# Kernel optimization log

Hardware: AMD Instinct MI355X
Metric: run time of the kernel (lower is better)

Reference implementation:

```python
import jax, jax.numpy as jnp
import numpy as np

B, S, H, L, NH, OUT = 64, 512, 512, 2, 8, 1
HD = H // NH
SKIP_INTERVAL = 2
EPS = 1e-5


def ln(x, g, b):
    m = x.mean(-1, keepdims=True)
    v = x.var(-1, keepdims=True)
    return (x - m) / jnp.sqrt(v + EPS) * g + b


def setup_inputs() -> dict:
    key = jax.random.key(0)
    ks = iter(jax.random.split(key, 64))
    def nrm(shape, s=0.02):
        return jax.random.normal(next(ks), shape, jnp.float32) * s
    inp = {
        'x': jax.random.normal(next(ks), (B, S, H), jnp.float32),
        # stacked per-layer LSTM params (input_size == hidden_size == H)
        'Wi': nrm((L, 4 * H, H)), 'bi': jnp.zeros((L, 4 * H), jnp.float32).at[:, H:2 * H].set(1.0),
        'Wh': nrm((L, 4 * H, H)), 'bh': jnp.zeros((L, 4 * H), jnp.float32).at[:, H:2 * H].set(1.0),
        'g_in': jnp.ones((L, 4 * H), jnp.float32), 'b_in': jnp.zeros((L, 4 * H), jnp.float32),
        'g_hid': jnp.ones((L, 4 * H), jnp.float32), 'b_hid': jnp.zeros((L, 4 * H), jnp.float32),
        'g_cell': jnp.ones((L, H), jnp.float32), 'b_cell': jnp.zeros((L, H), jnp.float32),
        # highway per layer
        'hw_Wt': nrm((L, H, H)), 'hw_bt': jnp.zeros((L, H), jnp.float32),
        'hw_Wc': nrm((L, H, H)), 'hw_bc': jnp.full((L, H), -1.0, jnp.float32),
        'hw_Wh': nrm((L, H, H)), 'hw_bh': jnp.zeros((L, H), jnp.float32),
        # attention
        'Wq': nrm((H, H)), 'bq': jnp.zeros((H,), jnp.float32),
        'Wk': nrm((H, H)), 'bk': jnp.zeros((H,), jnp.float32),
        'Wv': nrm((H, H)), 'bv': jnp.zeros((H,), jnp.float32),
        'Wo': nrm((H, H)), 'bo': jnp.zeros((H,), jnp.float32),
        'att_g': jnp.ones((H,), jnp.float32), 'att_b': jnp.zeros((H,), jnp.float32),
        # output norm + projection head
        'on_g': jnp.ones((H,), jnp.float32), 'on_b': jnp.zeros((H,), jnp.float32),
        'Wp1': nrm((H // 2, H)), 'bp1': jnp.zeros((H // 2,), jnp.float32),
        'Wp2': nrm((OUT, H // 2)), 'bp2': jnp.zeros((OUT,), jnp.float32),
    }
    return inp


def _forward(x, Wi, bi, Wh, bh, g_in, b_in, g_hid, b_hid, g_cell, b_cell,
             hw_Wt, hw_bt, hw_Wc, hw_bc, hw_Wh, hw_bh,
             Wq, bq, Wk, bk, Wv, bv, Wo, bo, att_g, att_b,
             on_g, on_b, Wp1, bp1, Wp2, bp2):
    def lstm_layer(seq, l):
        # precompute input projection + its LayerNorm for all timesteps: [B,S,4H]
        ip = ln(jnp.einsum('bsh,gh->bsg', seq, Wi[l]) + bi[l], g_in[l], b_in[l])
        def step(carry, ip_t):
            h, c = carry
            hp = ln(h @ Wh[l].T + bh[l], g_hid[l], b_hid[l])
            i_, f_, g_, o_ = jnp.split(ip_t + hp, 4, axis=-1)
            c = jax.nn.sigmoid(f_) * c + jax.nn.sigmoid(i_) * jnp.tanh(g_)
            h = jax.nn.sigmoid(o_) * jnp.tanh(ln(c, g_cell[l], b_cell[l]))
            return (h, c), h
        h0 = jnp.zeros((seq.shape[0], H), seq.dtype)
        _, hs = jax.lax.scan(step, (h0, h0), jnp.swapaxes(ip, 0, 1))
        return jnp.swapaxes(hs, 0, 1)  # [B,S,H]

    seq = x
    for l in range(L):
        h_seq = lstm_layer(seq, l)
        # highway network
        tg = jax.nn.sigmoid(h_seq @ hw_Wt[l].T + hw_bt[l])
        cg = jax.nn.sigmoid(h_seq @ hw_Wc[l].T + hw_bc[l])
        tr = jax.nn.relu(h_seq @ hw_Wh[l].T + hw_bh[l])
        h_seq = tg * tr + cg * h_seq
        # skip connection every SKIP_INTERVAL layers
        if l > 0 and (l + 1) % SKIP_INTERVAL == 0:
            h_seq = h_seq + seq
        seq = h_seq

    # multi-head self-attention with residual + LayerNorm
    def heads(y):
        return jnp.swapaxes(y.reshape(B, S, NH, HD), 1, 2)  # [B,NH,S,HD]
    q = heads(seq @ Wq.T + bq)
    k = heads(seq @ Wk.T + bk)
    v = heads(seq @ Wv.T + bv)
    scale = 1.0 / float(np.sqrt(HD))
    scores = jnp.einsum('bnqd,bnkd->bnqk', q, k) * scale
    aw = jax.nn.softmax(scores, axis=-1)
    ctx = jnp.einsum('bnqk,bnkd->bnqd', aw, v)
    ctx = jnp.swapaxes(ctx, 1, 2).reshape(B, S, H)
    att = ln(ctx @ Wo.T + bo + seq, att_g, att_b)

    # last timestep -> output norm -> MLP head
    last = ln(att[:, -1], on_g, on_b)
    hmid = jax.nn.relu(last @ Wp1.T + bp1)
    return hmid @ Wp2.T + bp2  # [B, OUT]


def reference(x, Wi, bi, Wh, bh, g_in, b_in, g_hid, b_hid, g_cell, b_cell,
              hw_Wt, hw_bt, hw_Wc, hw_bc, hw_Wh, hw_bh,
              Wq, bq, Wk, bk, Wv, bv, Wo, bo, att_g, att_b,
              on_g, on_b, Wp1, bp1, Wp2, bp2):
    return _forward(x, Wi, bi, Wh, bh, g_in, b_in, g_hid, b_hid, g_cell, b_cell,
                    hw_Wt, hw_bt, hw_Wc, hw_bc, hw_Wh, hw_bh,
                    Wq, bq, Wk, bk, Wv, bv, Wo, bo, att_g, att_b,
                    on_g, on_b, Wp1, bp1, Wp2, bp2)
```

## Files before the change

### kernel.cpp

```cpp
#include <hip/hip_runtime.h>

#define EPS_LN 1e-5f

static constexpr int Bn  = 64;
static constexpr int Sn  = 512;
static constexpr int Hn  = 512;
static constexpr int G4n = 2048;

typedef unsigned int uint32;
typedef unsigned long long uint64;
typedef _Float16 h2v __attribute__((ext_vector_type(2)));
typedef _Float16 h8v __attribute__((ext_vector_type(8)));
typedef float f4v __attribute__((ext_vector_type(4)));

__device__ __forceinline__ float sigf(float x)     { return 1.0f / (1.0f + __expf(-x)); }
__device__ __forceinline__ float tanhfast(float x) { return 1.0f - 2.0f / (1.0f + __expf(2.0f * x)); }

__device__ __forceinline__ float dot2h(uint32 w, uint32 h, float acc) {
#if defined(__has_builtin)
#if __has_builtin(__builtin_amdgcn_fdot2)
  return __builtin_amdgcn_fdot2(__builtin_bit_cast(h2v, w), __builtin_bit_cast(h2v, h), acc, false);
#define DOT2_DONE 1
#endif
#endif
#ifndef DOT2_DONE
  h2v wv = __builtin_bit_cast(h2v, w);
  h2v hv = __builtin_bit_cast(h2v, h);
  return acc + (float)wv.x * (float)hv.x + (float)wv.y * (float)hv.y;
#endif
}
__device__ __forceinline__ uint32 packh2(float a, float b) {
  h2v v; v.x = (_Float16)a; v.y = (_Float16)b;
  return __builtin_bit_cast(uint32, v);
}

__device__ __forceinline__ float blk_sum(float v, float* sm, int tid) {
#pragma unroll
  for (int o = 32; o; o >>= 1) v += __shfl_down(v, o, 64);
  __syncthreads();
  if ((tid & 63) == 0) sm[tid >> 6] = v;
  __syncthreads();
  return sm[0] + sm[1] + sm[2] + sm[3];
}
__device__ __forceinline__ float blk_max(float v, float* sm, int tid) {
#pragma unroll
  for (int o = 32; o; o >>= 1) v = fmaxf(v, __shfl_down(v, o, 64));
  __syncthreads();
  if ((tid & 63) == 0) sm[tid >> 6] = v;
  __syncthreads();
  return fmaxf(fmaxf(sm[0], sm[1]), fmaxf(sm[2], sm[3]));
}

__device__ __forceinline__ void blk_sum4_w8(float& a, float& b, float& c, float& d,
                                            float* sm, int tid) {
#pragma unroll
  for (int o = 32; o; o >>= 1) {
    a += __shfl_down(a, o, 64);
    b += __shfl_down(b, o, 64);
    c += __shfl_down(c, o, 64);
    d += __shfl_down(d, o, 64);
  }
  __syncthreads();
  if ((tid & 63) == 0) {
    float4 v; v.x = a; v.y = b; v.z = c; v.w = d;
    *(float4*)&sm[(tid >> 6) * 4] = v;
  }
  __syncthreads();
  float ra = 0.f, rb = 0.f, rc = 0.f, rd = 0.f;
#pragma unroll
  for (int w = 0; w < 8; ++w) {
    float4 v = *(const float4*)&sm[w * 4];
    ra += v.x; rb += v.y; rc += v.z; rd += v.w;
  }
  a = ra; b = rb; c = rc; d = rd;
}

__global__ __launch_bounds__(256) void wh_pack_k(
    const float* __restrict__ Wh, uint32* __restrict__ WhP)
{
  __shared__ float tile[32][33];
  const int l = blockIdx.z;
  const int k0 = blockIdx.x * 32;
  const int n0 = blockIdx.y * 32;
  const int row = threadIdx.x >> 5, col = threadIdx.x & 31;
  const float* src = Wh + (long)l * G4n * Hn;
  uint32* dst = WhP + (long)l * 256 * G4n;
#pragma unroll
  for (int rr = 0; rr < 4; ++rr) {
    int nn = row + rr * 8;
    tile[nn][col] = src[(long)(n0 + nn) * Hn + k0 + col];
  }
  __syncthreads();
#pragma unroll
  for (int rr = 0; rr < 2; ++rr) {
    int kpl = row + rr * 8;
    int kp = (k0 >> 1) + kpl;
    dst[(long)kp * G4n + n0 + col] = packh2(tile[col][2*kpl], tile[col][2*kpl+1]);
  }
}

__global__ void init_zbuf_k(uint64* zbuf)
{
  long i = (long)blockIdx.x * 512 + threadIdx.x;
  zbuf[i] = 0ULL;
}

__global__ __launch_bounds__(256) void gemm_ip_k(
    const float* __restrict__ A,
    const float* __restrict__ Bw,
    const float* __restrict__ bias,
    uint32* __restrict__ C,
    int s0)
{
  __shared__ __align__(16) uint32 Ast[128 * 20];
  __shared__ __align__(16) uint32 Bst[128 * 20];
  const int tid = threadIdx.x;
  const long m0 = (long)blockIdx.y * 128;
  const int n0 = blockIdx.x * 128;

  const int rt = tid >> 1;
  const int hf = tid & 1;
  const long r  = m0 + rt;
  const long b  = r & 63;
  const long sl = r >> 6;
  const float* Arow = A + (b * Sn + s0 + sl) * Hn + hf * 16;
  const float* Brow = Bw + (long)(n0 + rt) * 512 + hf * 16;
  const int sbase = rt * 20 + hf * 8;

  const int w  = tid >> 6;
  const int l  = tid & 63;
  const int lr = l & 15;
  const int lk = (l >> 4) * 4;

  f4v acc[8][2];
#pragma unroll
  for (int ct = 0; ct < 8; ++ct)
#pragma unroll
    for (int mt = 0; mt < 2; ++mt) {
      acc[ct][mt][0] = 0.f; acc[ct][mt][1] = 0.f;
      acc[ct][mt][2] = 0.f; acc[ct][mt][3] = 0.f;
    }

  float4 pa0 = *(const float4*)(Arow + 0);
  float4 pa1 = *(const float4*)(Arow + 4);
  float4 pa2 = *(const float4*)(Arow + 8);
  float4 pa3 = *(const float4*)(Arow + 12);
  float4 pb0 = *(const float4*)(Brow + 0);
  float4 pb1 = *(const float4*)(Brow + 4);
  float4 pb2 = *(const float4*)(Brow + 8);
  float4 pb3 = *(const float4*)(Brow + 12);

  for (int ks = 0; ks < 16; ++ks) {
    __syncthreads();
    {
      uint4 ua0, ua1, ub0, ub1;
      ua0.x = packh2(pa0.x, pa0.y); ua0.y = packh2(pa0.z, pa0.w);
      ua0.z = packh2(pa1.x, pa1.y); ua0.w = packh2(pa1.z, pa1.w);
      ua1.x = packh2(pa2.x, pa2.y); ua1.y = packh2(pa2.z, pa2.w);
      ua1.z = packh2(pa3.x, pa3.y); ua1.w = packh2(pa3.z, pa3.w);
      ub0.x = packh2(pb0.x, pb0.y); ub0.y = packh2(pb0.z, pb0.w);
      ub0.z = packh2(pb1.x, pb1.y); ub0.w = packh2(pb1.z, pb1.w);
      ub1.x = packh2(pb2.x, pb2.y); ub1.y = packh2(pb2.z, pb2.w);
      ub1.z = packh2(pb3.x, pb3.y); ub1.w = packh2(pb3.z, pb3.w);
      *(uint4*)&Ast[sbase]     = ua0;
      *(uint4*)&Ast[sbase + 4] = ua1;
      *(uint4*)&Bst[sbase]     = ub0;
      *(uint4*)&Bst[sbase + 4] = ub1;
    }
    __syncthreads();
    if (ks + 1 < 16) {
      const int ko = (ks + 1) * 32;
      pa0 = *(const float4*)(Arow + ko + 0);
      pa1 = *(const float4*)(Arow + ko + 4);
      pa2 = *(const float4*)(Arow + ko + 8);
      pa3 = *(const float4*)(Arow + ko + 12);
      pb0 = *(const float4*)(Brow + ko + 0);
      pb1 = *(const float4*)(Brow + ko + 4);
      pb2 = *(const float4*)(Brow + ko + 8);
      pb3 = *(const float4*)(Brow + ko + 12);
    }
    uint4 aw0 = *(const uint4*)&Ast[(w*32 + lr) * 20 + lk];
    uint4 aw1 = *(const uint4*)&Ast[(w*32 + 16 + lr) * 20 + lk];
    h8v af0 = __builtin_bit_cast(h8v, aw0);
    h8v af1 = __builtin_bit_cast(h8v, aw1);
#pragma unroll
    for (int ct = 0; ct < 8; ++ct) {
      uint4 bw4 = *(const uint4*)&Bst[(ct*16 + lr) * 20 + lk];
      h8v bf = __builtin_bit_cast(h8v, bw4);
      acc[ct][0] = __builtin_amdgcn_mfma_f32_16x16x32_f16(af0, bf, acc[ct][0], 0, 0, 0);
      acc[ct][1] = __builtin_amdgcn_mfma_f32_16x16x32_f16(af1, bf, acc[ct][1], 0, 0, 0);
    }
  }

  float bs[8];
#pragma unroll
  for (int ct = 0; ct < 8; ++ct) bs[ct] = bias[n0 + ct*16 + lr];
  const long mbase = m0 + w*32 + (l >> 4) * 4;
#pragma unroll
  for (int ct = 0; ct < 8; ++ct) {
    const int cp = (n0 + ct*16 + lr) >> 1;
#pragma unroll
    for (int mt = 0; mt < 2; ++mt) {
#pragma unroll
      for (int j = 0; j < 4; ++j) {
        float v = acc[ct][mt][j] + bs[ct];
        float vh = __shfl_xor(v, 1, 64);
        if (!(l & 1)) {
          const long m = mbase + mt*16 + j;
          C[m * 1024 + cp] = packh2(v, vh);
        }
      }
    }
  }
}

__global__ __launch_bounds__(256) void ipstats_k(
    const uint32* __restrict__ X, float* __restrict__ st)
{
  const long row = blockIdx.x;
  const uint32* xr = X + row * 1024;
  const int tid = threadIdx.x;
  __shared__ float sm[4];
  uint4 w = *(const uint4*)(xr + tid*4);
  h2v a = __builtin_bit_cast(h2v, w.x);
  h2v b = __builtin_bit_cast(h2v, w.y);
  h2v c = __builtin_bit_cast(h2v, w.z);
  h2v d = __builtin_bit_cast(h2v, w.w);
  float v[8] = {(float)a.x,(float)a.y,(float)b.x,(float)b.y,
                (float)c.x,(float)c.y,(float)d.x,(float)d.y};
  float s1 = 0.f, s2 = 0.f;
#pragma unroll
  for (int i = 0; i < 8; ++i) { s1 += v[i]; s2 += v[i]*v[i]; }
  s1 = blk_sum(s1, sm, tid);
  s2 = blk_sum(s2, sm, tid);
  if (tid == 0) {
    const float mean = s1 * (1.f/2048.f);
    const float rstd = rsqrtf(s2 * (1.f/2048.f) - mean*mean + EPS_LN);
    st[row*2]     = mean;
    st[row*2 + 1] = rstd;
  }
}

__global__ __launch_bounds__(256) void hw_fused_k(
    const float* __restrict__ A,
    const float* __restrict__ Wt, const float* __restrict__ bt,
    const float* __restrict__ Wc, const float* __restrict__ bc,
    const float* __restrict__ Wh3, const float* __restrict__ bh3,
    float* __restrict__ seqout,
    int skip)
{
  __shared__ __align__(16) uint32 Ah[8][128];
  __shared__ __align__(16) uint32 Bh[3][8][68];
  const int tid = threadIdx.x;
  const long m0 = (long)blockIdx.y * 128;
  const int n0 = blockIdx.x * 64;
  const int tx = tid & 7;
  const int ty = tid >> 3;
  const int lrow = tid >> 1;
  const int lc0  = (tid & 1) * 8;
  const int kbA  = (tid & 1) * 4;
  const int brow = tid >> 2;
  const int bk0  = (tid & 3) * 4;
  const int kbB  = (tid & 3) * 2;

  float accT[4][8], accC[4][8], accH[4][8];
#pragma unroll
  for (int i = 0; i < 4; ++i)
#pragma unroll
    for (int j = 0; j < 8; ++j) { accT[i][j] = 0.f; accC[i][j] = 0.f; accH[i][j] = 0.f; }

  const float* Arow = A + (m0 + lrow) * 512;
  const long boff = (long)(n0 + brow) * 512 + bk0;

  float4 a0 = *(const float4*)(Arow + lc0);
  float4 a1 = *(const float4*)(Arow + lc0 + 4);
  float4 wt4 = *(const float4*)(Wt  + boff);
  float4 wc4 = *(const float4*)(Wc  + boff);
  float4 wh4 = *(const float4*)(Wh3 + boff);

  for (int k0 = 0; k0 < 512; k0 += 16) {
    __syncthreads();
    Ah[kbA+0][lrow] = packh2(a0.x, a0.y);
    Ah[kbA+1][lrow] = packh2(a0.z, a0.w);
    Ah[kbA+2][lrow] = packh2(a1.x, a1.y);
    Ah[kbA+3][lrow] = packh2(a1.z, a1.w);
    Bh[0][kbB+0][brow] = packh2(wt4.x, wt4.y);
    Bh[0][kbB+1][brow] = packh2(wt4.z, wt4.w);
    Bh[1][kbB+0][brow] = packh2(wc4.x, wc4.y);
    Bh[1][kbB+1][brow] = packh2(wc4.z, wc4.w);
    Bh[2][kbB+0][brow] = packh2(wh4.x, wh4.y);
    Bh[2][kbB+1][brow] = packh2(wh4.z, wh4.w);
    __syncthreads();
    if (k0 + 16 < 512) {
      a0 = *(const float4*)(Arow + k0 + 16 + lc0);
      a1 = *(const float4*)(Arow + k0 + 16 + lc0 + 4);
      wt4 = *(const float4*)(Wt  + boff + k0 + 16);
      wc4 = *(const float4*)(Wc  + boff + k0 + 16);
      wh4 = *(const float4*)(Wh3 + boff + k0 + 16);
    }
#pragma unroll
    for (int kp = 0; kp < 8; ++kp) {
      uint32 a4[4];
      *(uint4*)&a4[0] = *(const uint4*)&Ah[kp][ty*4];
      {
        uint32 b8[8];
        *(uint4*)&b8[0] = *(const uint4*)&Bh[0][kp][tx*8];
        *(uint4*)&b8[4] = *(const uint4*)&Bh[0][kp][tx*8+4];
#pragma unroll
        for (int i = 0; i < 4; ++i)
#pragma unroll
          for (int j = 0; j < 8; ++j) accT[i][j] = dot2h(a4[i], b8[j], accT[i][j]);
      }
      {
        uint32 b8[8];
        *(uint4*)&b8[0] = *(const uint4*)&Bh[1][kp][tx*8];
        *(uint4*)&b8[4] = *(const uint4*)&Bh[1][kp][tx*8+4];
#pragma unroll
        for (int i = 0; i < 4; ++i)
#pragma unroll
          for (int j = 0; j < 8; ++j) accC[i][j] = dot2h(a4[i], b8[j], accC[i][j]);
      }
      {
        uint32 b8[8];
        *(uint4*)&b8[0] = *(const uint4*)&Bh[2][kp][tx*8];
        *(uint4*)&b8[4] = *(const uint4*)&Bh[2][kp][tx*8+4];
#pragma unroll
        for (int i = 0; i < 4; ++i)
#pragma unroll
          for (int j = 0; j < 8; ++j) accH[i][j] = dot2h(a4[i], b8[j], accH[i][j]);
      }
    }
  }

  float btr[8], bcr[8], bhr[8];
#pragma unroll
  for (int j = 0; j < 8; ++j) {
    btr[j] = bt[n0 + tx*8 + j];
    bcr[j] = bc[n0 + tx*8 + j];
    bhr[j] = bh3[n0 + tx*8 + j];
  }
#pragma unroll
  for (int i = 0; i < 4; ++i) {
    const long m = m0 + ty*4 + i;
    const float* hrow = A + m * 512 + n0 + tx*8;
    float* srow = seqout + m * 512 + n0 + tx*8;
    float4 h0 = *(const float4*)hrow;
    float4 h1 = *(const float4*)(hrow + 4);
    float hv[8] = {h0.x,h0.y,h0.z,h0.w,h1.x,h1.y,h1.z,h1.w};
    float sv[8] = {0,0,0,0,0,0,0,0};
    if (skip) {
      float4 s0 = *(const float4*)srow;
      float4 s1 = *(const float4*)(srow + 4);
      sv[0]=s0.x; sv[1]=s0.y; sv[2]=s0.z; sv[3]=s0.w;
      sv[4]=s1.x; sv[5]=s1.y; sv[6]=s1.z; sv[7]=s1.w;
    }
    float o[8];
#pragma unroll
    for (int j = 0; j < 8; ++j) {
      const float t1 = accT[i][j] + btr[j];
      const float t2 = accC[i][j] + bcr[j];
      const float t3 = accH[i][j] + bhr[j];
      o[j] = sigf(t1) * fmaxf(t3, 0.f) + sigf(t2) * hv[j] + sv[j];
    }
    float4 o0, o1;
    o0.x=o[0]; o0.y=o[1]; o0.z=o[2]; o0.w=o[3];
    o1.x=o[4]; o1.y=o[5]; o1.z=o[6]; o1.w=o[7];
    *(float4*)srow = o0; *(float4*)(srow + 4) = o1;
  }
}

__global__ __launch_bounds__(256) void gemm_m64_k(
    const float* __restrict__ A, long lda,
    const float* __restrict__ Bw,
    const float* __restrict__ bias,
    float* __restrict__ P,
    int N, int K)
{
  __shared__ float As[64][64];
  __shared__ float Bs[64][64];
  const int tid = threadIdx.x;
  const int n0 = blockIdx.x * 64;
  const int kc = blockIdx.y;
  const int Kc = K / gridDim.y;
  const int tx = tid & 15, ty = tid >> 4;
  const int row = tid >> 2, q = tid & 3;
  float acc[4][4];
#pragma unroll
  for (int i = 0; i < 4; ++i)
#pragma unroll
    for (int j = 0; j < 4; ++j) acc[i][j] = 0.f;

  for (int k0 = kc * Kc; k0 < kc * Kc + Kc; k0 += 64) {
    float4 a[4], b[4];
#pragma unroll
    for (int c = 0; c < 4; ++c) {
      a[c] = *(const float4*)(A  + (long)row * lda       + k0 + q*16 + c*4);
      b[c] = *(const float4*)(Bw + (long)(n0 + row) * K  + k0 + q*16 + c*4);
    }
    __syncthreads();
#pragma unroll
    for (int c = 0; c < 4; ++c) {
      int kb = q*16 + c*4;
      As[kb+0][row]=a[c].x; As[kb+1][row]=a[c].y; As[kb+2][row]=a[c].z; As[kb+3][row]=a[c].w;
      Bs[kb+0][row]=b[c].x; Bs[kb+1][row]=b[c].y; Bs[kb+2][row]=b[c].z; Bs[kb+3][row]=b[c].w;
    }
    __syncthreads();
#pragma unroll
    for (int kk = 0; kk < 64; ++kk) {
      float4 av = *(const float4*)&As[kk][ty*4];
      float4 bv = *(const float4*)&Bs[kk][tx*4];
      float am[4] = {av.x, av.y, av.z, av.w};
      float bm[4] = {bv.x, bv.y, bv.z, bv.w};
#pragma unroll
      for (int i = 0; i < 4; ++i)
#pragma unroll
        for (int j = 0; j < 4; ++j) acc[i][j] += am[i] * bm[j];
    }
  }
#pragma unroll
  for (int i = 0; i < 4; ++i) {
    int m = ty*4 + i;
    float* pr = P + ((long)kc * 64 + m) * N + n0 + tx*4;
#pragma unroll
    for (int j = 0; j < 4; ++j) {
      float bb = bias ? bias[n0 + tx*4 + j] : 0.f;
      pr[j] = acc[i][j] + bb;
    }
  }
}

__global__ __launch_bounds__(512, 2) void lstm_seqz_k(
    const uint32* __restrict__ WhP,
    const float* __restrict__ bh,
    const uint32* __restrict__ ipc,
    const float* __restrict__ ipstats,
    const float* __restrict__ g_in, const float* __restrict__ b_in,
    const float* __restrict__ g_hid, const float* __restrict__ b_hid,
    const float* __restrict__ g_cell, const float* __restrict__ b_cell,
    float* __restrict__ hst, float* __restrict__ cst,
    float* __restrict__ hseq,
    uint64* __restrict__ zbuf,
    int t0, int nsteps, int gbase)
{
  const int blk = blockIdx.x;
  const int g   = blk & 31;
  const int kq  = blk >> 5;
  const int tid = threadIdx.x;
  const int b0  = g*2, b1 = g*2 + 1;
  const int r   = tid >> 1;
  const int kh  = tid & 1;
  __shared__ __align__(16) uint32 hp0[264];
  __shared__ __align__(16) uint32 hp1[264];
  __shared__ float sm[32];

  uint4 wreg[32];
  {
    const uint32* base = WhP + (long)(kh * 128) * 2048 + (kq*256 + r);
#pragma unroll
    for (int i = 0; i < 32; ++i) {
      wreg[i].x = base[(long)(4*i + 0) * 2048];
      wreg[i].y = base[(long)(4*i + 1) * 2048];
      wreg[i].z = base[(long)(4*i + 2) * 2048];
      wreg[i].w = base[(long)(4*i + 3) * 2048];
    }
  }

  float bhr[4], ghr[4], bhir[4], ginr[4], binr[4];
#pragma unroll
  for (int q = 0; q < 4; ++q) {
    bhr[q]  = bh[q*512 + tid];
    ghr[q]  = g_hid[q*512 + tid];
    bhir[q] = b_hid[q*512 + tid];
    ginr[q] = g_in[q*512 + tid];
    binr[q] = b_in[q*512 + tid];
  }
  const float gcv = g_cell[tid];
  const float bcv = b_cell[tid];
  float c0 = cst[b0*512 + tid];
  float c1 = cst[b1*512 + tid];
  float h0 = hst[b0*512 + tid];
  float h1 = hst[b1*512 + tid];

  {
    const float p0 = __shfl_xor(h0, 1, 64);
    const float p1 = __shfl_xor(h1, 1, 64);
    if (!(tid & 1)) {
      const int j = tid >> 1;
      const int jj = (j < 128) ? j : j + 4;
      hp0[jj] = packh2(h0, p0);
      hp1[jj] = packh2(h1, p1);
    }
  }
  __syncthreads();

  const long myword = (long)(kq*256 + r) * 2 + kh;
  const uint32* hb0 = hp0 + kh * 132;
  const uint32* hb1 = hp1 + kh * 132;

  for (int ts = 0; ts < nsteps; ++ts) {
    const int gstep = gbase + ts;
    const uint32 tagw = (uint32)gstep;
    uint64* zp = zbuf + (long)(gstep & 1) * 131072 + (long)g * 4096;

    const uint32* iprow0 = ipc + ((long)ts * 64 + b0) * 1024 + (tid >> 1);
    const uint32* iprow1 = ipc + ((long)ts * 64 + b1) * 1024 + (tid >> 1);
    const float2 st0 = *(const float2*)(ipstats + ((long)ts * 64 + b0) * 2);
    const float2 st1 = *(const float2*)(ipstats + ((long)ts * 64 + b1) * 2);
    float ip0[4], ip1[4];
#pragma unroll
    for (int q = 0; q < 4; ++q) {
      h2v v0 = __builtin_bit_cast(h2v, iprow0[q*256]);
      h2v v1 = __builtin_bit_cast(h2v, iprow1[q*256]);
      const float r0 = kh ? (float)v0.y : (float)v0.x;
      const float r1 = kh ? (float)v1.y : (float)v1.x;
      ip0[q] = (r0 - st0.x) * st0.y * ginr[q] + binr[q];
      ip1[q] = (r1 - st1.x) * st1.y * ginr[q] + binr[q];
    }

    float a0 = 0.f, a1 = 0.f;
#pragma unroll
    for (int i = 0; i < 32; ++i) {
      const uint4 w  = wreg[i];
      const uint4 hv0 = *(const uint4*)&hb0[4*i];
      const uint4 hv1 = *(const uint4*)&hb1[4*i];
      a0 = dot2h(w.x, hv0.x, a0); a0 = dot2h(w.y, hv0.y, a0);
      a0 = dot2h(w.z, hv0.z, a0); a0 = dot2h(w.w, hv0.w, a0);
      a1 = dot2h(w.x, hv1.x, a1); a1 = dot2h(w.y, hv1.y, a1);
      a1 = dot2h(w.z, hv1.z, a1); a1 = dot2h(w.w, hv1.w, a1);
    }
    a0 += __shfl_xor(a0, 1, 64);
    a1 += __shfl_xor(a1, 1, 64);

    {
      const float zval = kh ? a1 : a0;
      const uint64 w = ((uint64)tagw << 32) | (uint64)__builtin_bit_cast(uint32, zval);
      __hip_atomic_store(zp + myword, w, __ATOMIC_RELAXED, __HIP_MEMORY_SCOPE_AGENT);
    }

    float z0[4], z1[4];
    {
      uint64 v0[4], v1[4];
      int pend = 0xff;
      while (pend) {
#pragma unroll
        for (int q = 0; q < 4; ++q) {
          const long base = (long)(q*512 + tid) * 2;
          if (pend & (1 << q)) {
            uint64 w = __hip_atomic_load(zp + base, __ATOMIC_RELAXED, __HIP_MEMORY_SCOPE_AGENT);
            if ((uint32)(w >> 32) == tagw) { v0[q] = w; pend &= ~(1 << q); }
          }
          if (pend & (16 << q)) {
            uint64 w = __hip_atomic_load(zp + base + 1, __ATOMIC_RELAXED, __HIP_MEMORY_SCOPE_AGENT);
            if ((uint32)(w >> 32) == tagw) { v1[q] = w; pend &= ~(16 << q); }
          }
        }
        if (pend) __builtin_amdgcn_s_sleep(2);
      }
#pragma unroll
      for (int q = 0; q < 4; ++q) {
        z0[q] = __builtin_bit_cast(float, (uint32)v0[q]) + bhr[q];
        z1[q] = __builtin_bit_cast(float, (uint32)v1[q]) + bhr[q];
      }
    }

    float s10 = z0[0]+z0[1]+z0[2]+z0[3];
    float s20 = z0[0]*z0[0] + z0[1]*z0[1] + z0[2]*z0[2] + z0[3]*z0[3];
    float s11 = z1[0]+z1[1]+z1[2]+z1[3];
    float s21 = z1[0]*z1[0] + z1[1]*z1[1] + z1[2]*z1[2] + z1[3]*z1[3];
    blk_sum4_w8(s10, s20, s11, s21, sm, tid);
    const float m0 = s10 * (1.f/2048.f);
    const float r0 = rsqrtf(s20 * (1.f/2048.f) - m0*m0 + EPS_LN);
    const float m1 = s11 * (1.f/2048.f);
    const float r1 = rsqrtf(s21 * (1.f/2048.f) - m1*m1 + EPS_LN);

    const float gi0 = ip0[0] + (z0[0] - m0) * r0 * ghr[0] + bhir[0];
    const float gf0 = ip0[1] + (z0[1] - m0) * r0 * ghr[1] + bhir[1];
    const float gg0 = ip0[2] + (z0[2] - m0) * r0 * ghr[2] + bhir[2];
    const float go0 = ip0[3] + (z0[3] - m0) * r0 * ghr[3] + bhir[3];
    const float gi1 = ip1[0] + (z1[0] - m1) * r1 * ghr[0] + bhir[0];
    const float gf1 = ip1[1] + (z1[1] - m1) * r1 * ghr[1] + bhir[1];
    const float gg1 = ip1[2] + (z1[2] - m1) * r1 * ghr[2] + bhir[2];
    const float go1 = ip1[3] + (z1[3] - m1) * r1 * ghr[3] + bhir[3];

    c0 = sigf(gf0) * c0 + sigf(gi0) * tanhfast(gg0);
    c1 = sigf(gf1) * c1 + sigf(gi1) * tanhfast(gg1);

    float t10 = c0, t20 = c0*c0, t11 = c1, t21 = c1*c1;
    blk_sum4_w8(t10, t20, t11, t21, sm, tid);
    const float n0 = t10 * (1.f/512.f);
    const float q0r = rsqrtf(t20 * (1.f/512.f) - n0*n0 + EPS_LN);
    const float n1 = t11 * (1.f/512.f);
    const float q1r = rsqrtf(t21 * (1.f/512.f) - n1*n1 + EPS_LN);
    h0 = sigf(go0) * tanhfast((c0 - n0) * q0r * gcv + bcv);
    h1 = sigf(go1) * tanhfast((c1 - n1) * q1r * gcv + bcv);

    if (kq == 0) {
      hseq[((long)b0 * Sn + t0 + ts) * Hn + tid] = h0;
      hseq[((long)b1 * Sn + t0 + ts) * Hn + tid] = h1;
    }

    const float p0 = __shfl_xor(h0, 1, 64);
    const float p1 = __shfl_xor(h1, 1, 64);
    if (!(tid & 1)) {
      const int j = tid >> 1;
      const int jj = (j < 128) ? j : j + 4;
      hp0[jj] = packh2(h0, p0);
      hp1[jj] = packh2(h1, p1);
    }
    __syncthreads();
  }
  if (kq == 0) {
    hst[b0*512 + tid] = h0; hst[b1*512 + tid] = h1;
    cst[b0*512 + tid] = c0; cst[b1*512 + tid] = c1;
  }
}

__global__ void init_hc_k(float* h, float* c)
{
  int i = blockIdx.x * 256 + threadIdx.x;
  h[i] = 0.f; c[i] = 0.f;
}

__global__ __launch_bounds__(256) void qkh_k(
    const float* __restrict__ qlst, const float* __restrict__ Wk,
    const float* __restrict__ bk,
    float* __restrict__ qkh, float* __restrict__ qbk)
{
  const int hd = blockIdx.x, cg = blockIdx.y;
  const int b = threadIdx.x & 63, sc = threadIdx.x >> 6;
  const int col0 = cg * 128 + sc * 32;
  float qreg[64];
  const float* qp = qlst + b*512 + hd*64;
#pragma unroll
  for (int j4 = 0; j4 < 16; ++j4) {
    float4 v = *(const float4*)(qp + j4*4);
    qreg[j4*4+0]=v.x; qreg[j4*4+1]=v.y; qreg[j4*4+2]=v.z; qreg[j4*4+3]=v.w;
  }
  float acc[32];
#pragma unroll
  for (int c = 0; c < 32; ++c) acc[c] = 0.f;
  for (int j = 0; j < 64; ++j) {
    float qv = qreg[j];
    const float* wr = Wk + (long)(hd*64 + j)*512 + col0;
#pragma unroll
    for (int c4 = 0; c4 < 8; ++c4) {
      float4 w = *(const float4*)(wr + c4*4);
      acc[c4*4+0] = __builtin_fmaf(qv, w.x, acc[c4*4+0]);
      acc[c4*4+1] = __builtin_fmaf(qv, w.y, acc[c4*4+1]);
      acc[c4*4+2] = __builtin_fmaf(qv, w.z, acc[c4*4+2]);
      acc[c4*4+3] = __builtin_fmaf(qv, w.w, acc[c4*4+3]);
    }
  }
  float* op = qkh + ((long)b*8 + hd)*512 + col0;
#pragma unroll
  for (int c4 = 0; c4 < 8; ++c4) {
    float4 o;
    o.x = acc[c4*4+0]; o.y = acc[c4*4+1]; o.z = acc[c4*4+2]; o.w = acc[c4*4+3];
    *(float4*)(op + c4*4) = o;
  }
  if (cg == 0 && sc == 0) {
    float s = 0.f;
    for (int j = 0; j < 64; ++j) s += qreg[j] * bk[hd*64 + j];
    qbk[b*8 + hd] = s;
  }
}

__global__ __launch_bounds__(256) void attn2_k(
    const float* __restrict__ seq,
    const float* __restrict__ qkh,
    const float* __restrict__ qbk,
    float* __restrict__ u)
{
  const int b = blockIdx.x, hd = blockIdx.y, tid = threadIdx.x;
  __shared__ __align__(16) float qk[512];
  __shared__ float p[512];
  __shared__ float sm[4];
  qk[tid]       = qkh[((long)b*8 + hd)*512 + tid];
  qk[tid + 256] = qkh[((long)b*8 + hd)*512 + tid + 256];
  __syncthreads();
  const float bias = qbk[b*8 + hd];

  float loc[2]; float mx = -3.0e38f;
#pragma unroll
  for (int v = 0; v < 2; ++v) {
    int s = tid + v*256;
    const float4* sr = (const float4*)(seq + ((long)b*512 + s)*512);
    const float4* qv4 = (const float4*)qk;
    float d = 0.f;
    for (int k4 = 0; k4 < 128; ++k4) {
      float4 sv = sr[k4], qv = qv4[k4];
      d += sv.x*qv.x + sv.y*qv.y + sv.z*qv.z + sv.w*qv.w;
    }
    d = (d + bias) * 0.125f;
    loc[v] = d; mx = fmaxf(mx, d);
  }
  const float M = blk_max(mx, sm, tid);
  float sum = 0.f;
#pragma unroll
  for (int v = 0; v < 2; ++v) {
    int s = tid + v*256;
    float e = __expf(loc[v] - M);
    p[s] = e; sum += e;
  }
  const float SM = blk_sum(sum, sm, tid);
  const float inv = 1.f / SM;

  float u0 = 0.f, u1 = 0.f;
  for (int s = 0; s < 512; ++s) {
    float ps = p[s];
    const float* srow = seq + ((long)b*512 + s)*512;
    u0 = __builtin_fmaf(ps, srow[tid], u0);
    u1 = __builtin_fmaf(ps, srow[tid + 256], u1);
  }
  u[((long)b*8 + hd)*512 + tid]       = u0 * inv;
  u[((long)b*8 + hd)*512 + tid + 256] = u1 * inv;
}

__global__ __launch_bounds__(256) void ctxv_k(
    const float* __restrict__ u, const float* __restrict__ Wv,
    const float* __restrict__ bv, float* __restrict__ ctx)
{
  const int b = blockIdx.x, tid = threadIdx.x;
  __shared__ __align__(16) float ul[8*512];
  for (int i = tid; i < 4096; i += 256) ul[i] = u[(long)b*4096 + i];
  __syncthreads();
#pragma unroll
  for (int v = 0; v < 2; ++v) {
    int n = tid + v*256;
    int hd = n >> 6;
    const float4* wr = (const float4*)(Wv + (long)n*512);
    const float4* uv = (const float4*)&ul[hd*512];
    float acc = 0.f;
    for (int k4 = 0; k4 < 128; ++k4) {
      float4 w = wr[k4], x = uv[k4];
      acc += w.x*x.x + w.y*x.y + w.z*x.z + w.w*x.w;
    }
    ctx[b*512 + n] = acc + bv[n];
  }
}

__global__ __launch_bounds__(256) void head_k(
    const float* __restrict__ ctx,
    const float* __restrict__ Wo, const float* __restrict__ bo,
    const float* __restrict__ seq,
    const float* __restrict__ att_g, const float* __restrict__ att_b,
    const float* __restrict__ on_g, const float* __restrict__ on_b,
    const float* __restrict__ Wp1, const float* __restrict__ bp1,
    const float* __restrict__ Wp2, const float* __restrict__ bp2,
    float* __restrict__ out)
{
  const int b = blockIdx.x, tid = threadIdx.x;
  __shared__ __align__(16) float cs[512];
  __shared__ __align__(16) float buf[512];
  __shared__ float sm[4];
  cs[tid]       = ctx[b*512 + tid];
  cs[tid + 256] = ctx[b*512 + tid + 256];
  __syncthreads();

  const float* srow = seq + ((long)b*512 + 511) * 512;
  float o[2];
#pragma unroll
  for (int v = 0; v < 2; ++v) {
    int j = tid + v*256;
    const float4* w4 = (const float4*)(Wo + (long)j * 512);
    const float4* c4 = (const float4*)cs;
    float acc = 0.f;
    for (int kx = 0; kx < 128; ++kx) {
      float4 w = w4[kx], c = c4[kx];
      acc += w.x*c.x + w.y*c.y + w.z*c.z + w.w*c.w;
    }
    o[v] = acc + bo[j] + srow[j];
  }
  float s1 = o[0] + o[1], s2 = o[0]*o[0] + o[1]*o[1];
  s1 = blk_sum(s1, sm, tid); s2 = blk_sum(s2, sm, tid);
  float m1 = s1 * (1.f/512.f);
  float r1 = rsqrtf(s2 * (1.f/512.f) - m1*m1 + EPS_LN);
  float a[2];
#pragma unroll
  for (int v = 0; v < 2; ++v) {
    int j = tid + v*256;
    a[v] = (o[v] - m1) * r1 * att_g[j] + att_b[j];
  }
  s1 = a[0] + a[1]; s2 = a[0]*a[0] + a[1]*a[1];
  s1 = blk_sum(s1, sm, tid); s2 = blk_sum(s2, sm, tid);
  float m2 = s1 * (1.f/512.f);
  float r2 = rsqrtf(s2 * (1.f/512.f) - m2*m2 + EPS_LN);
#pragma unroll
  for (int v = 0; v < 2; ++v) {
    int j = tid + v*256;
    buf[j] = (a[v] - m2) * r2 * on_g[j] + on_b[j];
  }
  __syncthreads();

  const float4* w1 = (const float4*)(Wp1 + (long)tid * 512);
  const float4* b4 = (const float4*)buf;
  float acc = 0.f;
  for (int kx = 0; kx < 128; ++kx) {
    float4 w = w1[kx], c = b4[kx];
    acc += w.x*c.x + w.y*c.y + w.z*c.z + w.w*c.w;
  }
  float mid = fmaxf(acc + bp1[tid], 0.f);
  float contrib = mid * Wp2[tid];
  float tot = blk_sum(contrib, sm, tid);
  if (tid == 0) out[b] = tot + bp2[0];
}

extern "C" void kernel_launch(void* const* d_in, const int* in_sizes, int n_in,
                              void* d_out, int out_size, void* d_ws, size_t ws_size,
                              hipStream_t stream)
{
  const float* x     = (const float*)d_in[0];
  const float* Wi    = (const float*)d_in[1];
  const float* bi    = (const float*)d_in[2];
  const float* Wh    = (const float*)d_in[3];
  const float* bh    = (const float*)d_in[4];
  const float* g_in  = (const float*)d_in[5];
  const float* b_in  = (const float*)d_in[6];
  const float* g_hid = (const float*)d_in[7];
  const float* b_hid = (const float*)d_in[8];
  const float* g_cell= (const float*)d_in[9];
  const float* b_cell= (const float*)d_in[10];
  const float* hwWt  = (const float*)d_in[11];
  const float* hwbt  = (const float*)d_in[12];
  const float* hwWc  = (const float*)d_in[13];
  const float* hwbc  = (const float*)d_in[14];
  const float* hwWh  = (const float*)d_in[15];
  const float* hwbh  = (const float*)d_in[16];
  const float* Wq    = (const float*)d_in[17];
  const float* bq    = (const float*)d_in[18];
  const float* Wk    = (const float*)d_in[19];
  const float* bk    = (const float*)d_in[20];
  const float* Wv    = (const float*)d_in[21];
  const float* bv    = (const float*)d_in[22];
  const float* Wo    = (const float*)d_in[23];
  const float* bo    = (const float*)d_in[24];
  const float* att_g = (const float*)d_in[25];
  const float* att_b = (const float*)d_in[26];
  const float* on_g  = (const float*)d_in[27];
  const float* on_b  = (const float*)d_in[28];
  const float* Wp1   = (const float*)d_in[29];
  const float* bp1   = (const float*)d_in[30];
  const float* Wp2   = (const float*)d_in[31];
  const float* bp2   = (const float*)d_in[32];
  float* out = (float*)d_out;

  const long SEQF = (long)Bn * Sn * Hn;
  const long WHPF = 2L * 256 * G4n;
  const long ZBF  = 2L * 32 * 2048 * 2;
  const long wsF  = (long)(ws_size / 4);

  float* ws   = (float*)d_ws;
  float* seq  = ws;
  float* hseq = seq  + SEQF;
  uint32* WhP = (uint32*)(hseq + SEQF);
  uint64* zbuf = (uint64*)(hseq + SEQF + WHPF);
  float* hst  = hseq + SEQF + WHPF + 2*ZBF;
  float* cst  = hst  + 32768L;
  float* qlst = cst  + 32768L;
  float* ctx  = qlst + 32768L;
  float* qkh  = ctx  + 32768L;
  float* qbk  = qkh  + 262144L;
  float* uat  = qbk  + 1024L;
  float* ipstats = uat + 262144L;
  float* ipcF = ipstats + 65536L;
  uint32* ipc = (uint32*)ipcF;
  const long baseF = (ipcF - ws);

  int TCH = 512;
  while (TCH > 16 && baseF + (long)TCH * 64 * 1024 > wsF) TCH >>= 1;

  wh_pack_k<<<dim3(16, 64, 2), 256, 0, stream>>>(Wh, WhP);
  init_zbuf_k<<<512, 512, 0, stream>>>(zbuf);

  const int NCH = Sn / TCH;
  const int MROWS = TCH * 64;
  const int NMCH = (Bn * Sn) / MROWS;

  for (int l = 0; l < 2; ++l) {
    const float* seqin = (l == 0) ? x : seq;
    init_hc_k<<<128, 256, 0, stream>>>(hst, cst);
    for (int c = 0; c < NCH; ++c) {
      const int s0 = c * TCH;
      gemm_ip_k<<<dim3(16, TCH/2), 256, 0, stream>>>(seqin, Wi + (long)l*G4n*Hn, bi + l*G4n, ipc, s0);
      ipstats_k<<<TCH*64, 256, 0, stream>>>(ipc, ipstats);
      lstm_seqz_k<<<256, 512, 0, stream>>>(WhP + (long)l*256*G4n, bh + l*G4n, ipc, ipstats,
          g_in + l*G4n, b_in + l*G4n,
          g_hid + l*G4n, b_hid + l*G4n, g_cell + l*Hn, b_cell + l*Hn,
          hst, cst, hseq, zbuf, s0, TCH, l*Sn + s0 + 1);
    }
    for (int mc = 0; mc < NMCH; ++mc) {
      const long m0 = (long)mc * MROWS;
      hw_fused_k<<<dim3(8, MROWS/128), 256, 0, stream>>>(
          hseq + m0*512,
          hwWt + (long)l*Hn*Hn, hwbt + l*Hn,
          hwWc + (long)l*Hn*Hn, hwbc + l*Hn,
          hwWh + (long)l*Hn*Hn, hwbh + l*Hn,
          seq + m0*512, (l == 0) ? 0 : 1);
    }
  }

  gemm_m64_k<<<dim3(8, 1), 256, 0, stream>>>(seq + 511L*512, 512L*512, Wq, bq, qlst, 512, 512);
  qkh_k<<<dim3(8, 4), 256, 0, stream>>>(qlst, Wk, bk, qkh, qbk);
  attn2_k<<<dim3(64, 8), 256, 0, stream>>>(seq, qkh, qbk, uat);
  ctxv_k<<<64, 256, 0, stream>>>(uat, Wv, bv, ctx);
  head_k<<<64, 256, 0, stream>>>(ctx, Wo, bo, seq, att_g, att_b, on_g, on_b, Wp1, bp1, Wp2, bp2, out);
}
```

Baseline: 8.463 ms.

## Rewrite highway fused GEMM to use MFMA 16x16x32 f16 instructions

Replaces the scalar fdot2-based register-tiled GEMM in the highway kernel with a wave-level MFMA implementation. Each wave computes 32 rows by 64 columns for all three weight matrices. Operands are staged as fp16 in padded shared memory with a K step of 32. The register-prefetch double buffering is dropped, and the epilogue now uses scalar loads and stores per accumulator element instead of float4 vectors. The aim is higher matrix throughput, at the cost of less load/compute overlap and less coalesced epilogue memory access.

```diff
diff --git a/kernel.cpp b/kernel.cpp
--- a/kernel.cpp
+++ b/kernel.cpp
@@ -249,123 +249,127 @@
     float* __restrict__ seqout,
     int skip)
 {
-  __shared__ __align__(16) uint32 Ah[8][128];
-  __shared__ __align__(16) uint32 Bh[3][8][68];
+  __shared__ __align__(16) uint32 Ast[128 * 20];
+  __shared__ __align__(16) uint32 Bst[3 * 64 * 20];
   const int tid = threadIdx.x;
   const long m0 = (long)blockIdx.y * 128;
   const int n0 = blockIdx.x * 64;
-  const int tx = tid & 7;
-  const int ty = tid >> 3;
-  const int lrow = tid >> 1;
-  const int lc0  = (tid & 1) * 8;
-  const int kbA  = (tid & 1) * 4;
-  const int brow = tid >> 2;
-  const int bk0  = (tid & 3) * 4;
-  const int kbB  = (tid & 3) * 2;
-
-  float accT[4][8], accC[4][8], accH[4][8];
-#pragma unroll
-  for (int i = 0; i < 4; ++i)
-#pragma unroll
-    for (int j = 0; j < 8; ++j) { accT[i][j] = 0.f; accC[i][j] = 0.f; accH[i][j] = 0.f; }
-
-  const float* Arow = A + (m0 + lrow) * 512;
-  const long boff = (long)(n0 + brow) * 512 + bk0;
-
-  float4 a0 = *(const float4*)(Arow + lc0);
-  float4 a1 = *(const float4*)(Arow + lc0 + 4);
-  float4 wt4 = *(const float4*)(Wt  + boff);
-  float4 wc4 = *(const float4*)(Wc  + boff);
-  float4 wh4 = *(const float4*)(Wh3 + boff);
-
-  for (int k0 = 0; k0 < 512; k0 += 16) {
+
+  const int rt = tid >> 1;
+  const int hf = tid & 1;
+  const float* Arow = A + (m0 + rt) * 512 + hf * 16;
+  const int sbaseA = rt * 20 + hf * 8;
+
+  const int u1 = tid;
+  const int u2 = tid + 256;
+  const int m1_ = u1 >> 7, r1_ = (u1 >> 1) & 63, h1_ = u1 & 1;
+  const int m2_ = u2 >> 7, r2_ = (u2 >> 1) & 63, h2_ = u2 & 1;
+  const float* bsrc1 = (m1_ == 0 ? Wt : (m1_ == 1 ? Wc : Wh3)) + (long)(n0 + r1_) * 512 + h1_ * 16;
+  const float* bsrc2 = (m2_ == 0 ? Wt : (m2_ == 1 ? Wc : Wh3)) + (long)(n0 + r2_) * 512 + h2_ * 16;
+  const int sbaseB1 = m1_ * 1280 + r1_ * 20 + h1_ * 8;
+  const int sbaseB2 = m2_ * 1280 + r2_ * 20 + h2_ * 8;
+
+  const int w  = tid >> 6;
+  const int l  = tid & 63;
+  const int lr = l & 15;
+  const int lk = (l >> 4) * 4;
+
+  f4v acc[3][4][2];
+#pragma unroll
+  for (int mat = 0; mat < 3; ++mat)
+#pragma unroll
+    for (int nt = 0; nt < 4; ++nt)
+#pragma unroll
+      for (int mt = 0; mt < 2; ++mt) {
+        acc[mat][nt][mt][0] = 0.f; acc[mat][nt][mt][1] = 0.f;
+        acc[mat][nt][mt][2] = 0.f; acc[mat][nt][mt][3] = 0.f;
+      }
+
+  for (int ks = 0; ks < 16; ++ks) {
+    const int ko = ks * 32;
     __syncthreads();
-    Ah[kbA+0][lrow] = packh2(a0.x, a0.y);
-    Ah[kbA+1][lrow] = packh2(a0.z, a0.w);
-    Ah[kbA+2][lrow] = packh2(a1.x, a1.y);
-    Ah[kbA+3][lrow] = packh2(a1.z, a1.w);
-    Bh[0][kbB+0][brow] = packh2(wt4.x, wt4.y);
-    Bh[0][kbB+1][brow] = packh2(wt4.z, wt4.w);
-    Bh[1][kbB+0][brow] = packh2(wc4.x, wc4.y);
-    Bh[1][kbB+1][brow] = packh2(wc4.z, wc4.w);
-    Bh[2][kbB+0][brow] = packh2(wh4.x, wh4.y);
-    Bh[2][kbB+1][brow] = packh2(wh4.z, wh4.w);
+    {
+      float4 a0 = *(const float4*)(Arow + ko + 0);
+      float4 a1 = *(const float4*)(Arow + ko + 4);
+      float4 a2 = *(const float4*)(Arow + ko + 8);
+      float4 a3 = *(const float4*)(Arow + ko + 12);
+      uint4 ua0, ua1;
+      ua0.x = packh2(a0.x, a0.y); ua0.y = packh2(a0.z, a0.w);
+      ua0.z = packh2(a1.x, a1.y); ua0.w = packh2(a1.z, a1.w);
+      ua1.x = packh2(a2.x, a2.y); ua1.y = packh2(a2.z, a2.w);
+      ua1.z = packh2(a3.x, a3.y); ua1.w = packh2(a3.z, a3.w);
+      *(uint4*)&Ast[sbaseA]     = ua0;
+      *(uint4*)&Ast[sbaseA + 4] = ua1;
+    }
+    {
+      float4 b0 = *(const float4*)(bsrc1 + ko + 0);
+      float4 b1 = *(const float4*)(bsrc1 + ko + 4);
+      float4 b2 = *(const float4*)(bsrc1 + ko + 8);
+      float4 b3 = *(const float4*)(bsrc1 + ko + 12);
+      uint4 ub0, ub1;
+      ub0.x = packh2(b0.x, b0.y); ub0.y = packh2(b0.z, b0.w);
+      ub0.z = packh2(b1.x, b1.y); ub0.w = packh2(b1.z, b1.w);
+      ub1.x = packh2(b2.x, b2.y); ub1.y = packh2(b2.z, b2.w);
+      ub1.z = packh2(b3.x, b3.y); ub1.w = packh2(b3.z, b3.w);
+      *(uint4*)&Bst[sbaseB1]     = ub0;
+      *(uint4*)&Bst[sbaseB1 + 4] = ub1;
+    }
+    if (tid < 128) {
+      float4 b0 = *(const float4*)(bsrc2 + ko + 0);
+      float4 b1 = *(const float4*)(bsrc2 + ko + 4);
+      float4 b2 = *(const float4*)(bsrc2 + ko + 8);
+      float4 b3 = *(const float4*)(bsrc2 + ko + 12);
+      uint4 ub0, ub1;
+      ub0.x = packh2(b0.x, b0.y); ub0.y = packh2(b0.z, b0.w);
+      ub0.z = packh2(b1.x, b1.y); ub0.w = packh2(b1.z, b1.w);
+      ub1.x = packh2(b2.x, b2.y); ub1.y = packh2(b2.z, b2.w);
+      ub1.z = packh2(b3.x, b3.y); ub1.w = packh2(b3.z, b3.w);
+      *(uint4*)&Bst[sbaseB2]     = ub0;
+      *(uint4*)&Bst[sbaseB2 + 4] = ub1;
+    }
     __syncthreads();
-    if (k0 + 16 < 512) {
-      a0 = *(const float4*)(Arow + k0 + 16 + lc0);
-      a1 = *(const float4*)(Arow + k0 + 16 + lc0 + 4);
-      wt4 = *(const float4*)(Wt  + boff + k0 + 16);
-      wc4 = *(const float4*)(Wc  + boff + k0 + 16);
-      wh4 = *(const float4*)(Wh3 + boff + k0 + 16);
-    }
-#pragma unroll
-    for (int kp = 0; kp < 8; ++kp) {
-      uint32 a4[4];
-      *(uint4*)&a4[0] = *(const uint4*)&Ah[kp][ty*4];
-      {
-        uint32 b8[8];
-        *(uint4*)&b8[0] = *(const uint4*)&Bh[0][kp][tx*8];
-        *(uint4*)&b8[4] = *(const uint4*)&Bh[0][kp][tx*8+4];
-#pragma unroll
-        for (int i = 0; i < 4; ++i)
-#pragma unroll
-          for (int j = 0; j < 8; ++j) accT[i][j] = dot2h(a4[i], b8[j], accT[i][j]);
+
+    uint4 aw0 = *(const uint4*)&Ast[(w*32 + lr) * 20 + lk];
+    uint4 aw1 = *(const uint4*)&Ast[(w*32 + 16 + lr) * 20 + lk];
+    h8v af0 = __builtin_bit_cast(h8v, aw0);
+    h8v af1 = __builtin_bit_cast(h8v, aw1);
+#pragma unroll
+    for (int mat = 0; mat < 3; ++mat) {
+#pragma unroll
+      for (int nt = 0; nt < 4; ++nt) {
+        uint4 bw4 = *(const uint4*)&Bst[mat*1280 + (nt*16 + lr) * 20 + lk];
+        h8v bf = __builtin_bit_cast(h8v, bw4);
+        acc[mat][nt][0] = __builtin_amdgcn_mfma_f32_16x16x32_f16(af0, bf, acc[mat][nt][0], 0, 0, 0);
+        acc[mat][nt][1] = __builtin_amdgcn_mfma_f32_16x16x32_f16(af1, bf, acc[mat][nt][1], 0, 0, 0);
       }
-      {
-        uint32 b8[8];
-        *(uint4*)&b8[0] = *(const uint4*)&Bh[1][kp][tx*8];
-        *(uint4*)&b8[4] = *(const uint4*)&Bh[1][kp][tx*8+4];
-#pragma unroll
-        for (int i = 0; i < 4; ++i)
-#pragma unroll
-          for (int j = 0; j < 8; ++j) accC[i][j] = dot2h(a4[i], b8[j], accC[i][j]);
+    }
+  }
+
+  float bsT[4], bsC[4], bsH[4];
+#pragma unroll
+  for (int nt = 0; nt < 4; ++nt) {
+    const int col = n0 + nt*16 + lr;
+    bsT[nt] = bt[col];
+    bsC[nt] = bc[col];
+    bsH[nt] = bh3[col];
+  }
+  const long mbase = m0 + w*32 + (l >> 4) * 4;
+#pragma unroll
+  for (int nt = 0; nt < 4; ++nt) {
+    const int col = n0 + nt*16 + lr;
+#pragma unroll
+    for (int mt = 0; mt < 2; ++mt) {
+#pragma unroll
+      for (int j = 0; j < 4; ++j) {
+        const long m = mbase + mt*16 + j;
+        const float t1 = acc[0][nt][mt][j] + bsT[nt];
+        const float t2 = acc[1][nt][mt][j] + bsC[nt];
+        const float t3 = acc[2][nt][mt][j] + bsH[nt];
+        const float hvv = A[m * 512 + col];
+        const float svv = skip ? seqout[m * 512 + col] : 0.f;
+        seqout[m * 512 + col] = sigf(t1) * fmaxf(t3, 0.f) + sigf(t2) * hvv + svv;
       }
-      {
-        uint32 b8[8];
-        *(uint4*)&b8[0] = *(const uint4*)&Bh[2][kp][tx*8];
-        *(uint4*)&b8[4] = *(const uint4*)&Bh[2][kp][tx*8+4];
-#pragma unroll
-        for (int i = 0; i < 4; ++i)
-#pragma unroll
-          for (int j = 0; j < 8; ++j) accH[i][j] = dot2h(a4[i], b8[j], accH[i][j]);
-      }
-    }
-  }
-
-  float btr[8], bcr[8], bhr[8];
-#pragma unroll
-  for (int j = 0; j < 8; ++j) {
-    btr[j] = bt[n0 + tx*8 + j];
-    bcr[j] = bc[n0 + tx*8 + j];
-    bhr[j] = bh3[n0 + tx*8 + j];
-  }
-#pragma unroll
-  for (int i = 0; i < 4; ++i) {
-    const long m = m0 + ty*4 + i;
-    const float* hrow = A + m * 512 + n0 + tx*8;
-    float* srow = seqout + m * 512 + n0 + tx*8;
-    float4 h0 = *(const float4*)hrow;
-    float4 h1 = *(const float4*)(hrow + 4);
-    float hv[8] = {h0.x,h0.y,h0.z,h0.w,h1.x,h1.y,h1.z,h1.w};
-    float sv[8] = {0,0,0,0,0,0,0,0};
-    if (skip) {
-      float4 s0 = *(const float4*)srow;
-      float4 s1 = *(const float4*)(srow + 4);
-      sv[0]=s0.x; sv[1]=s0.y; sv[2]=s0.z; sv[3]=s0.w;
-      sv[4]=s1.x; sv[5]=s1.y; sv[6]=s1.z; sv[7]=s1.w;
-    }
-    float o[8];
-#pragma unroll
-    for (int j = 0; j < 8; ++j) {
-      const float t1 = accT[i][j] + btr[j];
-      const float t2 = accC[i][j] + bcr[j];
-      const float t3 = accH[i][j] + bhr[j];
-      o[j] = sigf(t1) * fmaxf(t3, 0.f) + sigf(t2) * hv[j] + sv[j];
-    }
-    float4 o0, o1;
-    o0.x=o[0]; o0.y=o[1]; o0.z=o[2]; o0.w=o[3];
-    o1.x=o[4]; o1.y=o[5]; o1.z=o[6]; o1.w=o[7];
-    *(float4*)srow = o0; *(float4*)(srow + 4) = o1;
+    }
   }
 }
 
```

New measurement: 7.928 ms. 6.3% less time.
